# Kernel optimization log

Measured on AMD Instinct MI355X. Metric: run time of the kernel, lower is better.

Reference implementation:

```python
import jax, jax.numpy as jnp
import numpy as np

N, L, C = 256, 256, 8
DEPTH = 4  # truncation depth; output channels = C + C^2 + ... + C^DEPTH = 4680


def _tp(a, b):
    # tensor product of flattened signature levels: [N, A] x [N, B] -> [N, A*B]
    n = a.shape[0]
    return (a[:, :, None] * b[:, None, :]).reshape(n, -1)


def _exp_levels(v, depth):
    # exp(v) in the truncated tensor algebra: level j = v^{\otimes j} / j!
    # v: [N, C]; returns tuple of [N, C^j] for j = 1..depth
    levels = [v]
    for j in range(2, depth + 1):
        levels.append(_tp(levels[-1], v) / j)
    return tuple(levels)


def _sig_forward(path, depth):
    # signature(path, depth, stream=False, basepoint=False, inverse=False, initial=None)
    # = exp(x2-x1) (x) exp(x3-x2) (x) ... (x) exp(xL - x_{L-1})
    n, l, c = path.shape
    dx = path[:, 1:] - path[:, :-1]  # [N, L-1, C] increments
    sig0 = _exp_levels(dx[:, 0], depth)

    def step(sig, v):
        # Chen's relation: new_m = sum_{j=0}^{m} sig_{m-j} (x) e_j  (sig_0 = e_0 = 1)
        e = _exp_levels(v, depth)
        new = []
        for m in range(1, depth + 1):
            t = sig[m - 1] + e[m - 1]
            for j in range(1, m):
                t = t + _tp(sig[m - j - 1], e[j - 1])
            new.append(t)
        return tuple(new), None

    xs = jnp.moveaxis(dx[:, 1:], 1, 0)  # [L-2, N, C] -- sequential recursion over stream
    sig, _ = jax.lax.scan(jax.checkpoint(step), sig0, xs)
    return jnp.concatenate(sig, axis=-1)  # [N, C + C^2 + ... + C^depth]


def setup_inputs() -> dict:
    key = jax.random.key(0)
    path = jax.random.normal(key, (N, L, C), dtype=jnp.float32)
    return {"path": path}


def reference(path):
    return _sig_forward(path, DEPTH)
```

## Files before the change

### kernel.cpp

```cpp
#include <hip/hip_runtime.h>


constexpr int N_SAMP = 256;
constexpr int L_LEN = 256;
constexpr int C_DIM = 8;
constexpr int OUT_PER = 8 + 64 + 512 + 4096;
constexpr int NSEG = 4;
constexpr int SIG_STRIDE = 4688;

__global__ __launch_bounds__(1024) void sig_kernel(const float* __restrict__ path,
                                                   float* __restrict__ out) {
    __shared__ float dx[(L_LEN - 1) * C_DIM];
    __shared__ float sig[NSEG][SIG_STRIDE];

    const int n = blockIdx.x;
    const int tid = threadIdx.x;

    const float* p = path + (size_t)n * L_LEN * C_DIM;
    if (tid < 1020) {
        float2 a = *(const float2*)(p + tid * 2);
        float2 b = *(const float2*)(p + tid * 2 + C_DIM);
        *(float2*)(&dx[tid * 2]) = make_float2(b.x - a.x, b.y - a.y);
    }
    __syncthreads();

    const int seg = tid >> 8;
    const int r = tid & 255;
    const int i = r >> 5;
    const int j = (r >> 2) & 7;
    const int k0 = (r & 3) * 2;

    const int t0 = seg * 64;
    const int tcnt = (seg == 3) ? 63 : 64;

    float acc[16];
#pragma unroll
    for (int m = 0; m < 16; ++m) acc[m] = 0.f;
    float s3a = 0.f, s3b = 0.f, s2 = 0.f, s1 = 0.f;

    constexpr float THIRD = 1.f / 3.f;

#pragma unroll 4
    for (int t = 0; t < tcnt; ++t) {
        const float* v = &dx[(t0 + t) * C_DIM];
        float vv[8];
#pragma unroll
        for (int c = 0; c < 8; ++c) vv[c] = v[c];
        float vi = v[i];
        float vj = v[j];
        float2 vk = *(const float2*)(v + k0);
        float vk0 = vk.x, vk1 = vk.y;

        float c4 = fmaf(vj * THIRD, fmaf(0.25f, vi, s1), s2);
        float c3 = fmaf(vj * 0.5f, fmaf(THIRD, vi, s1), s2);
        float f0 = fmaf(c4, 0.5f * vk0, s3a);
        float f1 = fmaf(c4, 0.5f * vk1, s3b);

#pragma unroll
        for (int l = 0; l < 8; ++l) {
            acc[l] = fmaf(f0, vv[l], acc[l]);
            acc[8 + l] = fmaf(f1, vv[l], acc[8 + l]);
        }
        s3a = fmaf(c3, vk0, s3a);
        s3b = fmaf(c3, vk1, s3b);
        s2 = fmaf(fmaf(0.5f, vi, s1), vj, s2);
        s1 += vi;
    }

    {
        float* sg = sig[seg];
        if ((r & 31) == 0) sg[i] = s1;
        if ((r & 3) == 0) sg[8 + i * 8 + j] = s2;
        *(float2*)(&sg[72 + r * 2]) = make_float2(s3a, s3b);
        float* s4 = sg + 584 + r * 16;
        *(float4*)(s4) = make_float4(acc[0], acc[1], acc[2], acc[3]);
        *(float4*)(s4 + 4) = make_float4(acc[4], acc[5], acc[6], acc[7]);
        *(float4*)(s4 + 8) = make_float4(acc[8], acc[9], acc[10], acc[11]);
        *(float4*)(s4 + 12) = make_float4(acc[12], acc[13], acc[14], acc[15]);
    }
    __syncthreads();

    const int i4 = tid >> 7;
    const int j4 = (tid >> 4) & 7;
    const int k4 = (tid >> 1) & 7;
    const int l0 = (tid & 1) * 4;
    const int ijk4 = tid >> 1;

    for (int b = 1; b < NSEG; ++b) {
        const float* A = sig[0];
        const float* B = sig[b];

        float a3 = A[72 + ijk4];
        float a2 = A[8 + i4 * 8 + j4];
        float a1 = A[i4];
        float c4v[4];
#pragma unroll
        for (int m = 0; m < 4; ++m) {
            int l = l0 + m;
            float t = A[584 + ijk4 * 8 + l] + B[584 + ijk4 * 8 + l];
            t = fmaf(a3, B[l], t);
            t = fmaf(a2, B[8 + k4 * 8 + l], t);
            t = fmaf(a1, B[72 + j4 * 64 + k4 * 8 + l], t);
            c4v[m] = t;
        }
        float n3 = 0.f, n2 = 0.f, n1 = 0.f;
        if (tid < 512) {
            int ii = tid >> 6, jj = (tid >> 3) & 7, kk = tid & 7;
            n3 = A[72 + tid] + B[72 + tid];
            n3 = fmaf(A[8 + ii * 8 + jj], B[kk], n3);
            n3 = fmaf(A[ii], B[8 + jj * 8 + kk], n3);
        }
        if (tid < 64) {
            int ii = tid >> 3, jj = tid & 7;
            n2 = A[8 + tid] + B[8 + tid] + A[ii] * B[jj];
        }
        if (tid < 8) n1 = A[tid] + B[tid];
        __syncthreads();

        float* W = sig[0];
#pragma unroll
        for (int m = 0; m < 4; ++m) W[584 + ijk4 * 8 + l0 + m] = c4v[m];
        if (tid < 512) W[72 + tid] = n3;
        if (tid < 64) W[8 + tid] = n2;
        if (tid < 8) W[tid] = n1;
        __syncthreads();
    }

    float* o = out + (size_t)n * OUT_PER;
    for (int idx = tid; idx < OUT_PER; idx += 1024) o[idx] = sig[0][idx];
}

extern "C" void kernel_launch(void* const* d_in, const int* in_sizes, int n_in,
                              void* d_out, int out_size, void* d_ws, size_t ws_size,
                              hipStream_t stream) {
    const float* path = (const float*)d_in[0];
    float* out = (float*)d_out;
    sig_kernel<<<N_SAMP, 1024, 0, stream>>>(path, out);
}
```

Before: 67.81 us.

## Split stream into eight segments and merge via double shared buffers

Splits the 255 increments into 8 segments of 32 steps handled by 128 threads each, instead of 4 segments of 64 steps. Each thread now owns 32 level-4 accumulators instead of 16. Only two signature buffers stay in shared memory: later segments write their result into Y just before it is folded into X. This halves the sequential scan length and shrinks shared memory, at the cost of more registers per thread and seven serial Chen merges with extra barriers instead of three.

```diff
diff --git a/kernel.cpp b/kernel.cpp
--- a/kernel.cpp
+++ b/kernel.cpp
@@ -5,13 +5,13 @@
 constexpr int L_LEN = 256;
 constexpr int C_DIM = 8;
 constexpr int OUT_PER = 8 + 64 + 512 + 4096;
-constexpr int NSEG = 4;
-constexpr int SIG_STRIDE = 4688;
+constexpr int NSEG = 8;
 
 __global__ __launch_bounds__(1024) void sig_kernel(const float* __restrict__ path,
                                                    float* __restrict__ out) {
     __shared__ float dx[(L_LEN - 1) * C_DIM];
-    __shared__ float sig[NSEG][SIG_STRIDE];
+    __shared__ float X[OUT_PER];
+    __shared__ float Y[OUT_PER];
 
     const int n = blockIdx.x;
     const int tid = threadIdx.x;
@@ -24,19 +24,22 @@
     }
     __syncthreads();
 
-    const int seg = tid >> 8;
-    const int r = tid & 255;
-    const int i = r >> 5;
-    const int j = (r >> 2) & 7;
-    const int k0 = (r & 3) * 2;
+    const int seg = tid >> 7;
+    const int r = tid & 127;
+    const int i = r >> 4;
+    const int j = (r >> 1) & 7;
+    const bool khb = (r & 1);
 
-    const int t0 = seg * 64;
-    const int tcnt = (seg == 3) ? 63 : 64;
+    const int t0 = seg * 32;
+    const int tcnt = (seg == 7) ? 31 : 32;
 
-    float acc[16];
+    float acc[4][8];
 #pragma unroll
-    for (int m = 0; m < 16; ++m) acc[m] = 0.f;
-    float s3a = 0.f, s3b = 0.f, s2 = 0.f, s1 = 0.f;
+    for (int m = 0; m < 4; ++m)
+#pragma unroll
+        for (int l = 0; l < 8; ++l) acc[m][l] = 0.f;
+    float s3[4] = {0.f, 0.f, 0.f, 0.f};
+    float s2 = 0.f, s1 = 0.f;
 
     constexpr float THIRD = 1.f / 3.f;
 
@@ -48,86 +51,86 @@
         for (int c = 0; c < 8; ++c) vv[c] = v[c];
         float vi = v[i];
         float vj = v[j];
-        float2 vk = *(const float2*)(v + k0);
-        float vk0 = vk.x, vk1 = vk.y;
+        float vk[4];
+#pragma unroll
+        for (int m = 0; m < 4; ++m) vk[m] = khb ? vv[4 + m] : vv[m];
 
         float c4 = fmaf(vj * THIRD, fmaf(0.25f, vi, s1), s2);
         float c3 = fmaf(vj * 0.5f, fmaf(THIRD, vi, s1), s2);
-        float f0 = fmaf(c4, 0.5f * vk0, s3a);
-        float f1 = fmaf(c4, 0.5f * vk1, s3b);
 
 #pragma unroll
-        for (int l = 0; l < 8; ++l) {
-            acc[l] = fmaf(f0, vv[l], acc[l]);
-            acc[8 + l] = fmaf(f1, vv[l], acc[8 + l]);
+        for (int m = 0; m < 4; ++m) {
+            float f = fmaf(c4, 0.5f * vk[m], s3[m]);
+#pragma unroll
+            for (int l = 0; l < 8; ++l) acc[m][l] = fmaf(f, vv[l], acc[m][l]);
+            s3[m] = fmaf(c3, vk[m], s3[m]);
         }
-        s3a = fmaf(c3, vk0, s3a);
-        s3b = fmaf(c3, vk1, s3b);
         s2 = fmaf(fmaf(0.5f, vi, s1), vj, s2);
         s1 += vi;
     }
 
-    {
-        float* sg = sig[seg];
-        if ((r & 31) == 0) sg[i] = s1;
-        if ((r & 3) == 0) sg[8 + i * 8 + j] = s2;
-        *(float2*)(&sg[72 + r * 2]) = make_float2(s3a, s3b);
-        float* s4 = sg + 584 + r * 16;
-        *(float4*)(s4) = make_float4(acc[0], acc[1], acc[2], acc[3]);
-        *(float4*)(s4 + 4) = make_float4(acc[4], acc[5], acc[6], acc[7]);
-        *(float4*)(s4 + 8) = make_float4(acc[8], acc[9], acc[10], acc[11]);
-        *(float4*)(s4 + 12) = make_float4(acc[12], acc[13], acc[14], acc[15]);
-    }
+    auto write_sig = [&](float* sg) {
+        if ((r & 15) == 0) sg[i] = s1;
+        if (!khb) sg[8 + i * 8 + j] = s2;
+        *(float4*)(&sg[72 + r * 4]) = make_float4(s3[0], s3[1], s3[2], s3[3]);
+        float* s4p = sg + 584 + r * 32;
+#pragma unroll
+        for (int m = 0; m < 4; ++m) {
+            *(float4*)(s4p + m * 8) = make_float4(acc[m][0], acc[m][1], acc[m][2], acc[m][3]);
+            *(float4*)(s4p + m * 8 + 4) = make_float4(acc[m][4], acc[m][5], acc[m][6], acc[m][7]);
+        }
+    };
+
+    if (seg == 0) write_sig(X);
     __syncthreads();
 
-    const int i4 = tid >> 7;
-    const int j4 = (tid >> 4) & 7;
-    const int k4 = (tid >> 1) & 7;
+    const int ci = tid >> 7;
+    const int cj = (tid >> 4) & 7;
+    const int ck = (tid >> 1) & 7;
     const int l0 = (tid & 1) * 4;
     const int ijk4 = tid >> 1;
 
     for (int b = 1; b < NSEG; ++b) {
-        const float* A = sig[0];
-        const float* B = sig[b];
+        if (seg == b) write_sig(Y);
+        __syncthreads();
 
-        float a3 = A[72 + ijk4];
-        float a2 = A[8 + i4 * 8 + j4];
-        float a1 = A[i4];
+        float a3 = X[72 + ijk4];
+        float a2 = X[8 + ci * 8 + cj];
+        float a1 = X[ci];
         float c4v[4];
 #pragma unroll
         for (int m = 0; m < 4; ++m) {
             int l = l0 + m;
-            float t = A[584 + ijk4 * 8 + l] + B[584 + ijk4 * 8 + l];
-            t = fmaf(a3, B[l], t);
-            t = fmaf(a2, B[8 + k4 * 8 + l], t);
-            t = fmaf(a1, B[72 + j4 * 64 + k4 * 8 + l], t);
+            float t = X[584 + ijk4 * 8 + l] + Y[584 + ijk4 * 8 + l];
+            t = fmaf(a3, Y[l], t);
+            t = fmaf(a2, Y[8 + ck * 8 + l], t);
+            t = fmaf(a1, Y[72 + cj * 64 + ck * 8 + l], t);
             c4v[m] = t;
         }
         float n3 = 0.f, n2 = 0.f, n1 = 0.f;
         if (tid < 512) {
             int ii = tid >> 6, jj = (tid >> 3) & 7, kk = tid & 7;
-            n3 = A[72 + tid] + B[72 + tid];
-            n3 = fmaf(A[8 + ii * 8 + jj], B[kk], n3);
-            n3 = fmaf(A[ii], B[8 + jj * 8 + kk], n3);
+            n3 = X[72 + tid] + Y[72 + tid];
+            n3 = fmaf(X[8 + ii * 8 + jj], Y[kk], n3);
+            n3 = fmaf(X[ii], Y[8 + jj * 8 + kk], n3);
         }
         if (tid < 64) {
             int ii = tid >> 3, jj = tid & 7;
-            n2 = A[8 + tid] + B[8 + tid] + A[ii] * B[jj];
+            n2 = X[8 + tid] + Y[8 + tid] + X[ii] * Y[jj];
         }
-        if (tid < 8) n1 = A[tid] + B[tid];
+        if (tid < 8) n1 = X[tid] + Y[tid];
         __syncthreads();
 
-        float* W = sig[0];
 #pragma unroll
-        for (int m = 0; m < 4; ++m) W[584 + ijk4 * 8 + l0 + m] = c4v[m];
-        if (tid < 512) W[72 + tid] = n3;
-        if (tid < 64) W[8 + tid] = n2;
-        if (tid < 8) W[tid] = n1;
+        for (int m = 0; m < 4; ++m) X[584 + ijk4 * 8 + l0 + m] = c4v[m];
+        if (tid < 512) X[72 + tid] = n3;
+        if (tid < 64) X[8 + tid] = n2;
+        if (tid < 8) X[tid] = n1;
         __syncthreads();
     }
 
     float* o = out + (size_t)n * OUT_PER;
-    for (int idx = tid; idx < OUT_PER; idx += 1024) o[idx] = sig[0][idx];
+    for (int idx = tid; idx < OUT_PER; idx += 1024) o[idx] = X[idx];
 }
 
 extern "C" void kernel_launch(void* const* d_in, const int* in_sizes, int n_in,
```

New measurement: 101.4 us. +49.5%, slower.
